# Kernel optimization log

Measured on AMD Instinct MI355X. Metric: run time of the kernel, lower is better.

## Reference

```python
import jax, jax.numpy as jnp
import numpy as np

D_MODEL = 512
N_HEADS = 8
HEAD_DIM = D_MODEL // N_HEADS
STRIDE = 4
B, S = 2, 8192


def setup_inputs() -> dict:
    key = jax.random.key(0)
    ks = jax.random.split(key, 11)
    scale = 1.0 / np.sqrt(D_MODEL)
    inp = {
        'query': jax.random.normal(ks[0], (B, S, D_MODEL), jnp.float32),
        'key': jax.random.normal(ks[1], (B, S, D_MODEL), jnp.float32),
        'value': jax.random.normal(ks[2], (B, S, D_MODEL), jnp.float32),
        'Wq': jax.random.normal(ks[3], (D_MODEL, D_MODEL), jnp.float32) * scale,
        'bq': jnp.zeros((D_MODEL,), jnp.float32),
        'Wk': jax.random.normal(ks[4], (D_MODEL, D_MODEL), jnp.float32) * scale,
        'bk': jnp.zeros((D_MODEL,), jnp.float32),
        'Wv': jax.random.normal(ks[5], (D_MODEL, D_MODEL), jnp.float32) * scale,
        'bv': jnp.zeros((D_MODEL,), jnp.float32),
        'Wo': jax.random.normal(ks[6], (D_MODEL, D_MODEL), jnp.float32) * scale,
        'bo': jnp.zeros((D_MODEL,), jnp.float32),
    }
    return inp


def reference(query, key, value, Wq, bq, Wk, bk, Wv, bv, Wo, bo):
    b, s, _ = query.shape
    # Linear projections (torch nn.Linear: x @ W.T + b)
    Q = query @ Wq.T + bq
    K = key @ Wk.T + bk
    V = value @ Wv.T + bv
    # (B, H, S, Dh)
    Q = Q.reshape(b, s, N_HEADS, HEAD_DIM).transpose(0, 2, 1, 3)
    K = K.reshape(b, s, N_HEADS, HEAD_DIM).transpose(0, 2, 1, 3)
    V = V.reshape(b, s, N_HEADS, HEAD_DIM).transpose(0, 2, 1, 3)
    # Strided KV subsampling: (B, H, S/stride, Dh)
    K = K[:, :, ::STRIDE, :]
    V = V[:, :, ::STRIDE, :]
    # Dense attention over subsampled keys
    scores = jnp.einsum('bhqd,bhkd->bhqk', Q, K) / np.sqrt(HEAD_DIM).astype(np.float32)
    attn = jax.nn.softmax(scores, axis=-1)
    out = jnp.einsum('bhqk,bhkd->bhqd', attn, V)
    out = out.transpose(0, 2, 1, 3).reshape(b, s, D_MODEL)
    return out @ Wo.T + bo
```

## Files before the change

kernel.cpp:

```cpp
#include <hip/hip_runtime.h>

typedef unsigned short ushort;
typedef unsigned int uint;
typedef __bf16 bf16x8 __attribute__((ext_vector_type(8)));
typedef float f32x4 __attribute__((ext_vector_type(4)));

#define MFMA16(a, b, c) __builtin_amdgcn_mfma_f32_16x16x32_bf16((a), (b), (c), 0, 0, 0)


__device__ __forceinline__ ushort f2bs(float x) {
  __bf16 h = (__bf16)x;
  return __builtin_bit_cast(ushort, h);
}
__device__ __forceinline__ uint packbf2(float a, float b) {
  return (uint)f2bs(a) | ((uint)f2bs(b) << 16);
}
__device__ __forceinline__ float exp2fast(float x) {
#if __has_builtin(__builtin_amdgcn_exp2f)
  return __builtin_amdgcn_exp2f(x);
#else
  float r; asm("v_exp_f32 %0, %1" : "=v"(r) : "v"(x)); return r;
#endif
}
__device__ __forceinline__ void gload_lds16(const void* g, void* l) {
  __builtin_amdgcn_global_load_lds((const __attribute__((address_space(1))) void*)g,
                                   (__attribute__((address_space(3))) void*)l, 16, 0, 0);
}

__global__ __launch_bounds__(256) void cast_kernel(
    const float* __restrict__ q, const float* __restrict__ k, const float* __restrict__ v,
    const float* __restrict__ wq, const float* __restrict__ wk,
    const float* __restrict__ wv, const float* __restrict__ wo,
    ushort* __restrict__ qx, ushort* __restrict__ kx,
    ushort* __restrict__ vx, ushort* __restrict__ wx) {
  size_t gid = (size_t)blockIdx.x * 256 + threadIdx.x;
  const float* src;
  ushort* dst;
  if (gid < 1048576) {
    size_t f = gid * 8;
    src = q + f; dst = qx + f;
  } else if (gid < 1048576 + 262144) {
    size_t f = (gid - 1048576) * 8;
    size_t row = f >> 9, col = f & 511;
    size_t bb = row >> 11, s = row & 2047;
    src = k + ((bb * 8192 + s * 4) << 9) + col;
    dst = kx + f;
  } else if (gid < 1048576 + 524288) {
    size_t f = (gid - 1048576 - 262144) * 8;
    size_t row = f >> 9, col = f & 511;
    size_t bb = row >> 11, s = row & 2047;
    src = v + ((bb * 8192 + s * 4) << 9) + col;
    dst = vx + f;
  } else {
    size_t f = (gid - 1572864) * 8;
    int wsel = (int)(f >> 18);
    size_t o = f & 262143;
    src = (wsel == 0 ? wq : wsel == 1 ? wk : wsel == 2 ? wv : wo) + o;
    dst = wx + f;
  }
  float4 a = *(const float4*)(src);
  float4 c = *(const float4*)(src + 4);
  uint4 r;
  r.x = packbf2(a.x, a.y);
  r.y = packbf2(a.z, a.w);
  r.z = packbf2(c.x, c.y);
  r.w = packbf2(c.z, c.w);
  *(uint4*)dst = r;
}

template <int MODE>
__device__ __forceinline__ void gemm_body(
    const ushort* __restrict__ A, const ushort* __restrict__ W,
    const float* __restrict__ bias, ushort* __restrict__ outb,
    float* __restrict__ outf, ushort* __restrict__ outvt) {
  __shared__ ushort Al[2][4096];
  __shared__ ushort Bl[2][4096];

  int nwg = gridDim.x;
  int bid = blockIdx.x;
  int wg = (bid & 7) * (nwg >> 3) + (bid >> 3);
  int mt = wg >> 2, nt = wg & 3;
  size_t m0 = (size_t)mt << 7;
  int n0 = nt << 7;

  int tid = threadIdx.x;
  int wid = tid >> 6, lane = tid & 63;
  int r0 = lane & 15, g = lane >> 4;
  int wr = wid >> 1, wc = wid & 1;

  int idx0 = tid, idx1 = tid + 256;
  int rowA0 = idx0 >> 2, cb0 = (idx0 & 3) * 8;
  int rowA1 = idx1 >> 2, cb1 = (idx1 & 3) * 8;

  auto stage = [&](int buf, int kt) {
    int k0 = kt * 32;
    gload_lds16(A + (m0 + rowA0) * 512 + k0 + cb0, &Al[buf][idx0 * 8]);
    gload_lds16(A + (m0 + rowA1) * 512 + k0 + cb1, &Al[buf][idx1 * 8]);
    gload_lds16(W + (size_t)(n0 + rowA0) * 512 + k0 + cb0, &Bl[buf][idx0 * 8]);
    gload_lds16(W + (size_t)(n0 + rowA1) * 512 + k0 + cb1, &Bl[buf][idx1 * 8]);
  };

  f32x4 acc[4][4];
#pragma unroll
  for (int i = 0; i < 4; ++i)
#pragma unroll
    for (int j = 0; j < 4; ++j) acc[i][j] = (f32x4){0.f, 0.f, 0.f, 0.f};

  stage(0, 0);
  asm volatile("s_waitcnt vmcnt(0)" ::: "memory");
  __syncthreads();

  for (int kt = 0; kt < 16; ++kt) {
    int cur = kt & 1;
    if (kt < 15) stage(cur ^ 1, kt + 1);
    const ushort* ab = &Al[cur][(wr * 64 + r0) * 32 + g * 8];
    const ushort* bb = &Bl[cur][(wc * 64 + r0) * 32 + g * 8];
    bf16x8 af[4], bfv[4];
#pragma unroll
    for (int t = 0; t < 4; ++t) af[t] = *(const bf16x8*)(ab + t * 512);
#pragma unroll
    for (int t = 0; t < 4; ++t) bfv[t] = *(const bf16x8*)(bb + t * 512);
#pragma unroll
    for (int i = 0; i < 4; ++i)
#pragma unroll
      for (int j = 0; j < 4; ++j)
        acc[i][j] = MFMA16(af[i], bfv[j], acc[i][j]);
    asm volatile("s_waitcnt vmcnt(0)" ::: "memory");
    __syncthreads();
  }

  int colbase = n0 + wc * 64;
  float bv4[4];
#pragma unroll
  for (int j = 0; j < 4; ++j) bv4[j] = bias[colbase + j * 16 + r0];

#pragma unroll
  for (int i = 0; i < 4; ++i) {
    size_t rbase = m0 + (size_t)(wr * 64 + i * 16 + g * 4);
#pragma unroll
    for (int j = 0; j < 4; ++j) {
      int col = colbase + j * 16 + r0;
      if (MODE == 0) {
#pragma unroll
        for (int r = 0; r < 4; ++r)
          outb[(rbase + r) * 512 + col] = f2bs(acc[i][j][r] + bv4[j]);
      } else if (MODE == 2) {
#pragma unroll
        for (int r = 0; r < 4; ++r)
          outf[(rbase + r) * 512 + col] = acc[i][j][r] + bv4[j];
      } else {
        int b = (int)(rbase >> 11);
        int s = (int)(rbase & 2047);
        int h = col >> 6, d = col & 63;
        ushort us[4];
#pragma unroll
        for (int r = 0; r < 4; ++r) us[r] = f2bs(acc[i][j][r] + bv4[j]);
        uint2 pk;
        pk.x = (uint)us[0] | ((uint)us[1] << 16);
        pk.y = (uint)us[2] | ((uint)us[3] << 16);
        *(uint2*)(outvt + ((size_t)((b * 8 + h) * 64 + d)) * 2048 + s) = pk;
      }
    }
  }
}

template <int MODE>
__global__ __launch_bounds__(256) void gemm_bt(
    const ushort* __restrict__ A, const ushort* __restrict__ W,
    const float* __restrict__ bias, ushort* __restrict__ outb,
    float* __restrict__ outf, ushort* __restrict__ outvt) {
  gemm_body<MODE>(A, W, bias, outb, outf, outvt);
}

__global__ __launch_bounds__(256) void gemm_qkv(
    const ushort* __restrict__ qx, const ushort* __restrict__ kx,
    const ushort* __restrict__ vx,
    const ushort* __restrict__ wq, const ushort* __restrict__ wk,
    const ushort* __restrict__ wv,
    const float* __restrict__ bq, const float* __restrict__ bk,
    const float* __restrict__ bv,
    ushort* __restrict__ Q16, ushort* __restrict__ K16,
    ushort* __restrict__ VT16) {
  int y = blockIdx.y;
  if (y < 4) {
    size_t off = (size_t)y * 4096 * 512;
    gemm_body<0>(qx + off, wq, bq, Q16 + off, nullptr, nullptr);
  } else if (y == 4) {
    gemm_body<0>(kx, wk, bk, K16, nullptr, nullptr);
  } else {
    gemm_body<1>(vx, wv, bv, nullptr, nullptr, VT16);
  }
}

__global__ __launch_bounds__(256, 4) void attn_kernel(
    const ushort* __restrict__ Q, const ushort* __restrict__ K,
    const ushort* __restrict__ VT, ushort* __restrict__ O) {
  __shared__ ushort Kl[2][4096];
  __shared__ ushort Vl[2][4096];
  __shared__ ushort plds[4][1024];

  int bid = blockIdx.x;
  int wg = (bid & 7) * (gridDim.x >> 3) + (bid >> 3);
  int bh = wg >> 6;
  int qt = wg & 63;
  int b = bh >> 3, h = bh & 7;

  int tid = threadIdx.x, wid = tid >> 6, lane = tid & 63;
  int r0 = lane & 15, g = lane >> 4;
  int sw = r0 & 7;
  int q0 = qt * 128 + wid * 32;

  const float cs = 0.18033688011112042f;

  int srow = tid >> 3, su = tid & 7;
  const ushort* kstage = K + ((size_t)(b * 2048)) * 512 + h * 64;
  const ushort* vstage = VT + ((size_t)(bh * 64)) * 2048;

  auto stage = [&](int buf, int kv0) {
#pragma unroll
    for (int c = 0; c < 2; ++c) {
      int row = c * 32 + srow;
      int us = su ^ (row & 7);
      gload_lds16(kstage + (size_t)(kv0 + row) * 512 + us * 8,
                  &Kl[buf][(c * 256 + tid) * 8]);
    }
#pragma unroll
    for (int c = 0; c < 2; ++c) {
      int row = c * 32 + srow;
      int us = su ^ (row & 7);
      gload_lds16(vstage + (size_t)row * 2048 + kv0 + us * 8,
                  &Vl[buf][(c * 256 + tid) * 8]);
    }
  };

  bf16x8 qf[2][2];
#pragma unroll
  for (int st = 0; st < 2; ++st)
#pragma unroll
    for (int kk = 0; kk < 2; ++kk)
      qf[st][kk] = *(const bf16x8*)(Q + ((size_t)(b * 8192 + q0 + st * 16 + r0)) * 512 +
                                    h * 64 + kk * 32 + g * 8);

  f32x4 oacc[2][4];
#pragma unroll
  for (int st = 0; st < 2; ++st)
#pragma unroll
    for (int dt = 0; dt < 4; ++dt) oacc[st][dt] = (f32x4){0.f, 0.f, 0.f, 0.f};
  float lrun[2] = {0.f, 0.f};

  int koff0 = (g ^ sw) * 8;
  int koff1 = koff0 ^ 32;
  char* pw = (char*)&plds[wid][0];
  int swc = sw << 4;
  int pr0 = r0 * 128 + ((g ^ sw) << 4);
  int pr1 = pr0 ^ 64;

  stage(0, 0);
  asm volatile("s_waitcnt vmcnt(0)" ::: "memory");
  __syncthreads();

  for (int t = 0; t < 32; ++t) {
    int cur = t & 1;
    if (t < 31) stage(cur ^ 1, (t + 1) * 64);

    const ushort* kl = &Kl[cur][0];
    const ushort* vl = &Vl[cur][0];

    f32x4 s4[2][4];
#pragma unroll
    for (int ct = 0; ct < 4; ++ct) {
      const ushort* kp = kl + (ct * 16 + r0) * 64;
      bf16x8 k0 = *(const bf16x8*)(kp + koff0);
      bf16x8 k1 = *(const bf16x8*)(kp + koff1);
#pragma unroll
      for (int st = 0; st < 2; ++st) {
        f32x4 c = (f32x4){0.f, 0.f, 0.f, 0.f};
        c = MFMA16(k0, qf[st][0], c);
        c = MFMA16(k1, qf[st][1], c);
        s4[st][ct] = c;
      }
    }

#pragma unroll
    for (int st = 0; st < 2; ++st) {
      float ls = 0.f;
#pragma unroll
      for (int ct = 0; ct < 4; ++ct) {
        float p0 = exp2fast(s4[st][ct][0] * cs);
        float p1 = exp2fast(s4[st][ct][1] * cs);
        float p2 = exp2fast(s4[st][ct][2] * cs);
        float p3 = exp2fast(s4[st][ct][3] * cs);
        ls += (p0 + p1) + (p2 + p3);
        uint2 pk2;
        pk2.x = packbf2(p0, p1);
        pk2.y = packbf2(p2, p3);
        *(uint2*)(pw + r0 * 128 + ((ct * 32 + g * 8) ^ swc)) = pk2;
      }
      ls += __shfl_xor(ls, 16);
      ls += __shfl_xor(ls, 32);
      lrun[st] += ls;

#pragma unroll
      for (int ks = 0; ks < 2; ++ks) {
        bf16x8 pf = *(const bf16x8*)(pw + (ks == 0 ? pr0 : pr1));
        int vo = (ks == 0 ? koff0 : koff1);
#pragma unroll
        for (int dt = 0; dt < 4; ++dt) {
          bf16x8 vf = *(const bf16x8*)(vl + (dt * 16 + r0) * 64 + vo);
          oacc[st][dt] = MFMA16(pf, vf, oacc[st][dt]);
        }
      }
    }

    asm volatile("s_waitcnt vmcnt(0)" ::: "memory");
    __syncthreads();
  }

#pragma unroll
  for (int st = 0; st < 2; ++st) {
    float lr[4];
#pragma unroll
    for (int r = 0; r < 4; ++r) lr[r] = 1.f / __shfl(lrun[st], 4 * g + r);
    size_t rowb = (size_t)(b * 8192 + q0 + st * 16 + 4 * g);
#pragma unroll
    for (int dt = 0; dt < 4; ++dt)
#pragma unroll
      for (int r = 0; r < 4; ++r)
        O[(rowb + r) * 512 + h * 64 + dt * 16 + r0] = f2bs(oacc[st][dt][r] * lr[r]);
  }
}

extern "C" void kernel_launch(void* const* d_in, const int* in_sizes, int n_in,
                              void* d_out, int out_size, void* d_ws, size_t ws_size,
                              hipStream_t stream) {
  const float* query = (const float*)d_in[0];
  const float* key   = (const float*)d_in[1];
  const float* value = (const float*)d_in[2];
  const float* Wq = (const float*)d_in[3];
  const float* bq = (const float*)d_in[4];
  const float* Wk = (const float*)d_in[5];
  const float* bk = (const float*)d_in[6];
  const float* Wv = (const float*)d_in[7];
  const float* bv = (const float*)d_in[8];
  const float* Wo = (const float*)d_in[9];
  const float* bo = (const float*)d_in[10];
  float* out = (float*)d_out;

  ushort* ws  = (ushort*)d_ws;
  ushort* qx  = ws;
  ushort* kx  = qx + 8388608;
  ushort* vx  = kx + 2097152;
  ushort* wx  = vx + 2097152;
  ushort* Q16 = wx + 1048576;
  ushort* K16 = Q16 + 8388608;
  ushort* VT16 = K16 + 2097152;
  ushort* O16 = qx;

  cast_kernel<<<6656, 256, 0, stream>>>(query, key, value, Wq, Wk, Wv, Wo, qx, kx, vx, wx);
  gemm_qkv<<<dim3(128, 6), 256, 0, stream>>>(qx, kx, vx,
                                             wx + 0, wx + 262144, wx + 524288,
                                             bq, bk, bv, Q16, K16, VT16);
  attn_kernel<<<1024, 256, 0, stream>>>(Q16, K16, VT16, O16);
  gemm_bt<2><<<512, 256, 0, stream>>>(O16, wx + 786432, bo, nullptr, out, nullptr);
}
```

Before: 278.5 us.

## Fold softmax scale into Q projection, compute row sums via MFMA, use 512-thread attention blocks

The Q projection epilogue now multiplies by the softmax log2 scale, which removes a multiply per score in the attention loop. Row sums of P are accumulated with an extra MFMA against a vector of ones instead of per-lane adds and cross-lane shuffles. Attention blocks grow to 8 waves covering 256 queries, so each staged K/V tile is shared by twice as many waves and each thread issues one load per buffer. This costs some precision, because Q is rounded to bf16 after scaling and the sums now come from bf16 P values, and the larger blocks may lower occupancy.

```diff
diff --git a/kernel.cpp b/kernel.cpp
--- a/kernel.cpp
+++ b/kernel.cpp
@@ -134,6 +134,8 @@
 #pragma unroll
   for (int j = 0; j < 4; ++j) bv4[j] = bias[colbase + j * 16 + r0];
 
+  const float qs = 0.18033688011112042f;
+
 #pragma unroll
   for (int i = 0; i < 4; ++i) {
     size_t rbase = m0 + (size_t)(wr * 64 + i * 16 + g * 4);
@@ -144,6 +146,10 @@
 #pragma unroll
         for (int r = 0; r < 4; ++r)
           outb[(rbase + r) * 512 + col] = f2bs(acc[i][j][r] + bv4[j]);
+      } else if (MODE == 3) {
+#pragma unroll
+        for (int r = 0; r < 4; ++r)
+          outb[(rbase + r) * 512 + col] = f2bs((acc[i][j][r] + bv4[j]) * qs);
       } else if (MODE == 2) {
 #pragma unroll
         for (int r = 0; r < 4; ++r)
@@ -184,7 +190,7 @@
   int y = blockIdx.y;
   if (y < 4) {
     size_t off = (size_t)y * 4096 * 512;
-    gemm_body<0>(qx + off, wq, bq, Q16 + off, nullptr, nullptr);
+    gemm_body<3>(qx + off, wq, bq, Q16 + off, nullptr, nullptr);
   } else if (y == 4) {
     gemm_body<0>(kx, wk, bk, K16, nullptr, nullptr);
   } else {
@@ -192,45 +198,32 @@
   }
 }
 
-__global__ __launch_bounds__(256, 4) void attn_kernel(
+__global__ __launch_bounds__(512, 4) void attn_kernel(
     const ushort* __restrict__ Q, const ushort* __restrict__ K,
     const ushort* __restrict__ VT, ushort* __restrict__ O) {
   __shared__ ushort Kl[2][4096];
   __shared__ ushort Vl[2][4096];
-  __shared__ ushort plds[4][1024];
+  __shared__ ushort plds[8][1024];
 
   int bid = blockIdx.x;
   int wg = (bid & 7) * (gridDim.x >> 3) + (bid >> 3);
-  int bh = wg >> 6;
-  int qt = wg & 63;
+  int bh = wg >> 5;
+  int qt = wg & 31;
   int b = bh >> 3, h = bh & 7;
 
   int tid = threadIdx.x, wid = tid >> 6, lane = tid & 63;
   int r0 = lane & 15, g = lane >> 4;
   int sw = r0 & 7;
-  int q0 = qt * 128 + wid * 32;
-
-  const float cs = 0.18033688011112042f;
+  int q0 = qt * 256 + wid * 32;
 
   int srow = tid >> 3, su = tid & 7;
-  const ushort* kstage = K + ((size_t)(b * 2048)) * 512 + h * 64;
-  const ushort* vstage = VT + ((size_t)(bh * 64)) * 2048;
+  int sus = su ^ (srow & 7);
+  const ushort* kstage = K + ((size_t)(b * 2048)) * 512 + h * 64 + sus * 8;
+  const ushort* vstage = VT + ((size_t)(bh * 64 + srow)) * 2048 + sus * 8;
 
   auto stage = [&](int buf, int kv0) {
-#pragma unroll
-    for (int c = 0; c < 2; ++c) {
-      int row = c * 32 + srow;
-      int us = su ^ (row & 7);
-      gload_lds16(kstage + (size_t)(kv0 + row) * 512 + us * 8,
-                  &Kl[buf][(c * 256 + tid) * 8]);
-    }
-#pragma unroll
-    for (int c = 0; c < 2; ++c) {
-      int row = c * 32 + srow;
-      int us = su ^ (row & 7);
-      gload_lds16(vstage + (size_t)row * 2048 + kv0 + us * 8,
-                  &Vl[buf][(c * 256 + tid) * 8]);
-    }
+    gload_lds16(kstage + (size_t)(kv0 + srow) * 512, &Kl[buf][tid * 8]);
+    gload_lds16(vstage + kv0, &Vl[buf][tid * 8]);
   };
 
   bf16x8 qf[2][2];
@@ -241,12 +234,22 @@
       qf[st][kk] = *(const bf16x8*)(Q + ((size_t)(b * 8192 + q0 + st * 16 + r0)) * 512 +
                                     h * 64 + kk * 32 + g * 8);
 
+  bf16x8 ones;
+  {
+    ushort ob = 0x3F80;
+    __bf16 ov = __builtin_bit_cast(__bf16, ob);
+#pragma unroll
+    for (int i = 0; i < 8; ++i) ones[i] = ov;
+  }
+
   f32x4 oacc[2][4];
-#pragma unroll
-  for (int st = 0; st < 2; ++st)
+  f32x4 lacc[2];
+#pragma unroll
+  for (int st = 0; st < 2; ++st) {
+    lacc[st] = (f32x4){0.f, 0.f, 0.f, 0.f};
 #pragma unroll
     for (int dt = 0; dt < 4; ++dt) oacc[st][dt] = (f32x4){0.f, 0.f, 0.f, 0.f};
-  float lrun[2] = {0.f, 0.f};
+  }
 
   int koff0 = (g ^ sw) * 8;
   int koff1 = koff0 ^ 32;
@@ -283,22 +286,17 @@
 
 #pragma unroll
     for (int st = 0; st < 2; ++st) {
-      float ls = 0.f;
 #pragma unroll
       for (int ct = 0; ct < 4; ++ct) {
-        float p0 = exp2fast(s4[st][ct][0] * cs);
-        float p1 = exp2fast(s4[st][ct][1] * cs);
-        float p2 = exp2fast(s4[st][ct][2] * cs);
-        float p3 = exp2fast(s4[st][ct][3] * cs);
-        ls += (p0 + p1) + (p2 + p3);
+        float p0 = exp2fast(s4[st][ct][0]);
+        float p1 = exp2fast(s4[st][ct][1]);
+        float p2 = exp2fast(s4[st][ct][2]);
+        float p3 = exp2fast(s4[st][ct][3]);
         uint2 pk2;
         pk2.x = packbf2(p0, p1);
         pk2.y = packbf2(p2, p3);
         *(uint2*)(pw + r0 * 128 + ((ct * 32 + g * 8) ^ swc)) = pk2;
       }
-      ls += __shfl_xor(ls, 16);
-      ls += __shfl_xor(ls, 32);
-      lrun[st] += ls;
 
 #pragma unroll
       for (int ks = 0; ks < 2; ++ks) {
@@ -309,6 +307,7 @@
           bf16x8 vf = *(const bf16x8*)(vl + (dt * 16 + r0) * 64 + vo);
           oacc[st][dt] = MFMA16(pf, vf, oacc[st][dt]);
         }
+        lacc[st] = MFMA16(pf, ones, lacc[st]);
       }
     }
 
@@ -320,7 +319,7 @@
   for (int st = 0; st < 2; ++st) {
     float lr[4];
 #pragma unroll
-    for (int r = 0; r < 4; ++r) lr[r] = 1.f / __shfl(lrun[st], 4 * g + r);
+    for (int r = 0; r < 4; ++r) lr[r] = 1.f / lacc[st][r];
     size_t rowb = (size_t)(b * 8192 + q0 + st * 16 + 4 * g);
 #pragma unroll
     for (int dt = 0; dt < 4; ++dt)
@@ -360,6 +359,6 @@
   gemm_qkv<<<dim3(128, 6), 256, 0, stream>>>(qx, kx, vx,
                                              wx + 0, wx + 262144, wx + 524288,
                                              bq, bk, bv, Q16, K16, VT16);
-  attn_kernel<<<1024, 256, 0, stream>>>(Q16, K16, VT16, O16);
+  attn_kernel<<<512, 512, 0, stream>>>(Q16, K16, VT16, O16);
   gemm_bt<2><<<512, 256, 0, stream>>>(O16, wx + 786432, bo, nullptr, out, nullptr);
 }
```

Measured after the change: 271.3 us. 2.6% less time.
